# Kernel optimization log

Measured on AMD Instinct MI355X. Metric: run time of the kernel, lower is better.

## Reference

```python
import jax, jax.numpy as jnp
import numpy as np

B, D_IN, D_H, D_OUT, D_INT = 1024, 2048, 4096, 2048, 1024


def fwht(x):
    """Fast Walsh-Hadamard transform over a length-2^k vector (unnormalized),
    faithful to the torch chunk/cat butterfly loop."""
    n = x.shape[0]
    k = int(n).bit_length() - 1
    for i in range(k):
        y = x.reshape(2 ** i, 2, -1)        # split butterfly level i
        x = jnp.stack([y[:, 0] + y[:, 1], y[:, 0] - y[:, 1]], axis=1)
    return x.reshape(n)


def fastfood(V, BB, Pi, GG, DD):
    """fastfood_torched: pad -> B*x -> H -> permute -> G* -> H -> slice/scale."""
    LL = BB.shape[0]
    vpad = jnp.zeros((LL,), V.dtype).at[: V.shape[0]].set(V)
    m5 = fwht(fwht(BB * vpad)[Pi] * GG)
    divisor = jnp.sqrt(LL * jnp.sum(GG * GG))
    return m5[:DD] / (divisor * np.sqrt(float(DD) / LL))


def _ff_vars(key, DD):
    LL = 1 << int(np.ceil(np.log2(DD)))
    k1, k2, k3 = jax.random.split(key, 3)
    BB = jnp.where(jax.random.uniform(k1, (LL,)) < 0.5, -1.0, 1.0).astype(jnp.float32)
    Pi = jax.random.permutation(k2, LL).astype(jnp.int32)
    GG = jax.random.normal(k3, (LL,), dtype=jnp.float32)
    return BB, Pi, GG


def setup_inputs():
    key = jax.random.key(0)
    ks = jax.random.split(key, 8)
    x = jax.random.normal(ks[0], (B, D_IN), dtype=jnp.float32)
    V = jax.random.normal(ks[1], (D_INT,), dtype=jnp.float32) * 0.01
    W1_0 = jax.random.normal(ks[2], (D_H, D_IN), dtype=jnp.float32) * 0.02
    b1_0 = jnp.zeros((D_H,), jnp.float32)
    W2_0 = jax.random.normal(ks[3], (D_OUT, D_H), dtype=jnp.float32) * 0.02
    b2_0 = jnp.zeros((D_OUT,), jnp.float32)
    BB_W1, Pi_W1, GG_W1 = _ff_vars(ks[4], D_H * D_IN)
    BB_b1, Pi_b1, GG_b1 = _ff_vars(ks[5], D_H)
    BB_W2, Pi_W2, GG_W2 = _ff_vars(ks[6], D_OUT * D_H)
    BB_b2, Pi_b2, GG_b2 = _ff_vars(ks[7], D_OUT)
    return dict(x=x, V=V, W1_0=W1_0, b1_0=b1_0, W2_0=W2_0, b2_0=b2_0,
                BB_W1=BB_W1, Pi_W1=Pi_W1, GG_W1=GG_W1,
                BB_b1=BB_b1, Pi_b1=Pi_b1, GG_b1=GG_b1,
                BB_W2=BB_W2, Pi_W2=Pi_W2, GG_W2=GG_W2,
                BB_b2=BB_b2, Pi_b2=Pi_b2, GG_b2=GG_b2)


def reference(x, V, W1_0, b1_0, W2_0, b2_0,
              BB_W1, Pi_W1, GG_W1, BB_b1, Pi_b1, GG_b1,
              BB_W2, Pi_W2, GG_W2, BB_b2, Pi_b2, GG_b2):
    # Reconstruct each parameter: theta = theta0 + fastfood(V).view(shape)
    W1 = W1_0 + fastfood(V, BB_W1, Pi_W1, GG_W1, D_H * D_IN).reshape(D_H, D_IN)
    b1 = b1_0 + fastfood(V, BB_b1, Pi_b1, GG_b1, D_H)
    W2 = W2_0 + fastfood(V, BB_W2, Pi_W2, GG_W2, D_OUT * D_H).reshape(D_OUT, D_H)
    b2 = b2_0 + fastfood(V, BB_b2, Pi_b2, GG_b2, D_OUT)
    # Wrapped module forward (2-layer MLP)
    h = jax.nn.relu(x @ W1.T + b1)
    return h @ W2.T + b2
```

## Files before the change

### kernel.cpp

```cpp
#include <hip/hip_runtime.h>
#include <hip/hip_bf16.h>
#include <stdint.h>


typedef __attribute__((ext_vector_type(8))) short bf16x8;
typedef __attribute__((ext_vector_type(8))) short short8;
typedef __attribute__((ext_vector_type(4))) float f32x4;

__device__ __forceinline__ ushort f2bf(float f) {
  union { float f; uint32_t u; } v; v.f = f;
  return (ushort)((v.u + 0x7FFFu + ((v.u >> 16) & 1u)) >> 16);
}
__device__ __forceinline__ float bf2f(ushort u) {
  union { uint32_t u; float f; } v; v.u = (uint32_t)u << 16; return v.f;
}

__device__ __forceinline__ void gload_lds16(const void* g, void* l) {
  __builtin_amdgcn_global_load_lds(
      (const __attribute__((address_space(1))) void*)g,
      (__attribute__((address_space(3))) void*)l, 16, 0, 0);
}

__device__ __forceinline__ void wait_vm16() { asm volatile("s_waitcnt vmcnt(16)" ::: "memory"); }
__device__ __forceinline__ void wait_vm8()  { asm volatile("s_waitcnt vmcnt(8)"  ::: "memory"); }
__device__ __forceinline__ void wait_vm0()  { asm volatile("s_waitcnt vmcnt(0)"  ::: "memory"); }
__device__ __forceinline__ void wait_lgkm0(){ asm volatile("s_waitcnt lgkmcnt(0)" ::: "memory"); }
__device__ __forceinline__ void barrier_raw(){ asm volatile("s_barrier" ::: "memory"); }

template <int NN>
__device__ __forceinline__ void wht_inreg(float* v) {
#pragma unroll
  for (int h = 1; h < NN; h <<= 1)
#pragma unroll
    for (int g = 0; g < NN; g += (h << 1))
#pragma unroll
      for (int k = 0; k < h; ++k) {
        float a = v[g + k], b = v[g + k + h];
        v[g + k] = a + b; v[g + k + h] = a - b;
      }
}

__global__ __launch_bounds__(256) void prep(
    const float4* __restrict__ x4, ushort4* __restrict__ xb4,
    const float* __restrict__ V,
    const float* __restrict__ BBW1, const float* __restrict__ BBW2,
    float* __restrict__ t1, float* __restrict__ t2,
    const float* __restrict__ BBb1, const int* __restrict__ Pib1,
    const float* __restrict__ GGb1, const float* __restrict__ b10,
    const float* __restrict__ BBb2, const int* __restrict__ Pib2,
    const float* __restrict__ GGb2, const float* __restrict__ b20,
    float* __restrict__ ob1, float* __restrict__ ob2) {
  __shared__ float ts[1024];
  __shared__ float zs[4096];
  __shared__ float red[4];
  const int bid = blockIdx.x;
  const int tid = threadIdx.x;

  if (bid < 2048) {
    int i = bid * 256 + tid;
    float4 v = x4[i];
    ushort4 o;
    o.x = f2bf(v.x); o.y = f2bf(v.y); o.z = f2bf(v.z); o.w = f2bf(v.w);
    xb4[i] = o;
    return;
  }

  if (bid < 2050) {
    const int which = bid - 2048;
    const float* BB = which ? BBW2 : BBW1;
    float* t = which ? t2 : t1;
    for (int i = tid; i < 1024; i += 256) ts[i] = BB[i] * V[i];
    for (int st = 0; st < 10; ++st) {
      int half = 1 << st;
      __syncthreads();
      for (int j = tid; j < 512; j += 256) {
        int p = ((j >> st) << (st + 1)) | (j & (half - 1));
        float a = ts[p], b = ts[p + half];
        ts[p] = a + b; ts[p + half] = a - b;
      }
    }
    __syncthreads();
    for (int i = tid; i < 1024; i += 256) t[i] = ts[i];
    return;
  }

  {
    const int which = bid - 2050;
    const int L = which ? 2048 : 4096;
    const float* BB = which ? BBb2 : BBb1;
    const int* Pi = which ? Pib2 : Pib1;
    const float* GG = which ? GGb2 : GGb1;
    const float* b0 = which ? b20 : b10;
    float* ob = which ? ob2 : ob1;

    for (int i = tid; i < 1024; i += 256) ts[i] = BB[i] * V[i];
    for (int st = 0; st < 10; ++st) {
      int half = 1 << st;
      __syncthreads();
      for (int j = tid; j < 512; j += 256) {
        int p = ((j >> st) << (st + 1)) | (j & (half - 1));
        float a = ts[p], b = ts[p + half];
        ts[p] = a + b; ts[p + half] = a - b;
      }
    }
    __syncthreads();
    float gsum = 0.f;
    for (int i = tid; i < L; i += 256) {
      int pi = Pi[i];
      float g = GG[i];
      gsum += g * g;
      zs[i] = ts[pi & 1023] * g;
    }
    for (int o = 32; o > 0; o >>= 1) gsum += __shfl_down(gsum, o);
    if ((tid & 63) == 0) red[tid >> 6] = gsum;
    __syncthreads();
    float ssum = red[0] + red[1] + red[2] + red[3];
    for (int st = 0; (1 << st) < L; ++st) {
      int half = 1 << st;
      __syncthreads();
      for (int j = tid; j < (L >> 1); j += 256) {
        int p = ((j >> st) << (st + 1)) | (j & (half - 1));
        float a = zs[p], b = zs[p + half];
        zs[p] = a + b; zs[p + half] = a - b;
      }
    }
    __syncthreads();
    float scale = rsqrtf((float)L * ssum);
    for (int i = tid; i < L; i += 256) ob[i] = b0[i] + zs[i] * scale;
  }
}

__global__ __launch_bounds__(256) void build_z(
    const int* __restrict__ Pi1, const float* __restrict__ GG1,
    const int* __restrict__ Pi2, const float* __restrict__ GG2,
    const float* __restrict__ t1, const float* __restrict__ t2,
    ushort* __restrict__ z1, ushort* __restrict__ z2,
    float* __restrict__ partials) {
  __shared__ float ts[1024];
  __shared__ float red[4];
  const int tid = threadIdx.x;
  const int wsel = blockIdx.x >> 10;
  const int blk = blockIdx.x & 1023;
  const int* __restrict__ Pi = wsel ? Pi2 : Pi1;
  const float* __restrict__ GG = wsel ? GG2 : GG1;
  const float* t = wsel ? t2 : t1;
  ushort* __restrict__ z = wsel ? z2 : z1;
  const size_t base = (size_t)blk << 13;

  for (int i = tid; i < 1024; i += 256) ts[i] = t[i];

  int4 p4[8]; float4 g4[8];
  const int4* Pi4 = (const int4*)(Pi + base);
  const float4* GG4 = (const float4*)(GG + base);
#pragma unroll
  for (int q = 0; q < 4; ++q) {
    p4[2 * q]     = Pi4[(q << 9) + (tid << 1)];
    p4[2 * q + 1] = Pi4[(q << 9) + (tid << 1) + 1];
    g4[2 * q]     = GG4[(q << 9) + (tid << 1)];
    g4[2 * q + 1] = GG4[(q << 9) + (tid << 1) + 1];
  }
  __syncthreads();

  float gsum = 0.f;
#pragma unroll
  for (int q = 0; q < 4; ++q) {
    const int4 pa = p4[2 * q], pb = p4[2 * q + 1];
    const float4 ga = g4[2 * q], gb = g4[2 * q + 1];
    gsum += ga.x * ga.x + ga.y * ga.y + ga.z * ga.z + ga.w * ga.w
          + gb.x * gb.x + gb.y * gb.y + gb.z * gb.z + gb.w * gb.w;
    short8 o;
    o[0] = (short)f2bf(ts[pa.x & 1023] * ga.x);
    o[1] = (short)f2bf(ts[pa.y & 1023] * ga.y);
    o[2] = (short)f2bf(ts[pa.z & 1023] * ga.z);
    o[3] = (short)f2bf(ts[pa.w & 1023] * ga.w);
    o[4] = (short)f2bf(ts[pb.x & 1023] * gb.x);
    o[5] = (short)f2bf(ts[pb.y & 1023] * gb.y);
    o[6] = (short)f2bf(ts[pb.z & 1023] * gb.z);
    o[7] = (short)f2bf(ts[pb.w & 1023] * gb.w);
    *(short8*)(z + base + (q << 11) + (tid << 3)) = o;
  }
  for (int o2 = 32; o2 > 0; o2 >>= 1) gsum += __shfl_down(gsum, o2);
  if ((tid & 63) == 0) red[tid >> 6] = gsum;
  __syncthreads();
  if (tid == 0) partials[blockIdx.x] = red[0] + red[1] + red[2] + red[3];
}

__global__ __launch_bounds__(256) void wht13(
    const ushort* __restrict__ zz1, const ushort* __restrict__ zz2,
    ushort* __restrict__ inter1, ushort* __restrict__ inter2) {
  __shared__ float zs[8704];
  const int tid = threadIdx.x;
  const int wsel = blockIdx.x >> 10;
  const int blk = blockIdx.x & 1023;
  const ushort* __restrict__ z = wsel ? zz2 : zz1;
  ushort* __restrict__ inter = wsel ? inter2 : inter1;
  const size_t base = (size_t)blk << 13;

  float v[32];
#pragma unroll
  for (int j = 0; j < 4; ++j) {
    short8 d = *(const short8*)(z + base + (tid << 5) + (j << 3));
#pragma unroll
    for (int k = 0; k < 8; ++k) v[(j << 3) + k] = bf2f((ushort)d[k]);
  }
  wht_inreg<32>(v);
#pragma unroll
  for (int j = 0; j < 16; ++j) {
    float2 u; u.x = v[2 * j]; u.y = v[2 * j + 1];
    *(float2*)&zs[34 * tid + 2 * j] = u;
  }
  __syncthreads();

  {
    const int pb = (tid & 31) + 1088 * (tid >> 5);
#pragma unroll
    for (int r = 0; r < 32; ++r) v[r] = zs[pb + 34 * r];
    wht_inreg<32>(v);
#pragma unroll
    for (int r = 0; r < 32; ++r) zs[pb + 34 * r] = v[r];
  }
  __syncthreads();

  {
    const int pc = 4 * tid + 2 * (tid >> 3);
    float w[4][8];
#pragma unroll
    for (int r = 0; r < 8; ++r) {
      float2 u0 = *(const float2*)&zs[pc + 1088 * r];
      float2 u1 = *(const float2*)&zs[pc + 1088 * r + 2];
      w[0][r] = u0.x; w[1][r] = u0.y; w[2][r] = u1.x; w[3][r] = u1.y;
    }
#pragma unroll
    for (int k = 0; k < 4; ++k) wht_inreg<8>(w[k]);
    ushort* op = inter + base + 4 * tid;
#pragma unroll
    for (int r = 0; r < 8; ++r) {
      short4 o;
      o.x = (short)f2bf(w[0][r]); o.y = (short)f2bf(w[1][r]);
      o.z = (short)f2bf(w[2][r]); o.w = (short)f2bf(w[3][r]);
      *(short4*)&op[r << 10] = o;
    }
  }
}

__global__ __launch_bounds__(512) void ff_pass2(
    const ushort* __restrict__ inter1, const ushort* __restrict__ inter2,
    const float* __restrict__ W01, const float* __restrict__ W02,
    const float* __restrict__ partials,
    ushort* __restrict__ W1b, ushort* __restrict__ W2b) {
  __shared__ ushort tile[1024][34];
  __shared__ float red[8];
  const int tid = threadIdx.x;
  const int wsel = blockIdx.x >> 8;
  const int cb = (blockIdx.x & 255) << 5;
  const ushort* inter = wsel ? inter2 : inter1;
  const float* W0 = wsel ? W02 : W01;
  ushort* Wb = wsel ? W2b : W1b;

  float s = partials[(wsel << 10) + tid] + partials[(wsel << 10) + tid + 512];
  for (int o = 32; o > 0; o >>= 1) s += __shfl_down(s, o);
  if ((tid & 63) == 0) red[tid >> 6] = s;

  const int p = tid & 15;
  const int g = tid >> 4;
  const ushort* ip = inter + ((size_t)(g << 5) << 13) + cb + (p << 1);
  float va[32], vb[32];
#pragma unroll
  for (int r = 0; r < 32; ++r) {
    ushort2 u = *(const ushort2*)(ip + ((size_t)r << 13));
    va[r] = bf2f(u.x); vb[r] = bf2f(u.y);
  }
  wht_inreg<32>(va);
  wht_inreg<32>(vb);
#pragma unroll
  for (int r = 0; r < 32; ++r) {
    ushort2 u; u.x = f2bf(va[r]); u.y = f2bf(vb[r]);
    *(ushort2*)&tile[(g << 5) + r][p << 1] = u;
  }
  __syncthreads();
  float ssum = 0.f;
#pragma unroll
  for (int k = 0; k < 8; ++k) ssum += red[k];
  const float sc = rsqrtf(8388608.f * ssum);

  float wa[32], wb[32];
#pragma unroll
  for (int r = 0; r < 32; ++r) {
    ushort2 u = *(const ushort2*)&tile[g + (r << 5)][p << 1];
    wa[r] = bf2f(u.x); wb[r] = bf2f(u.y);
  }
  wht_inreg<32>(wa);
  wht_inreg<32>(wb);
#pragma unroll
  for (int r = 0; r < 32; ++r) {
    size_t m = (((size_t)(g + (r << 5))) << 13) + cb + (p << 1);
    float2 w0 = *(const float2*)(W0 + m);
    ushort2 u;
    u.x = f2bf(wa[r] * sc + w0.x);
    u.y = f2bf(wb[r] * sc + w0.y);
    *(ushort2*)(Wb + m) = u;
  }
}

template <int EPI, int NT>
__global__ __launch_bounds__(256) void gemm_bt(
    const ushort* __restrict__ A, const ushort* __restrict__ B,
    const float* __restrict__ bias, ushort* __restrict__ Cb, float* __restrict__ Cf,
    int M, int N, int K) {
  __shared__ ushort As[4][8192];
  __shared__ ushort Bs[4][8192];
  const int tid = threadIdx.x;
  const int w = tid >> 6, l = tid & 63;
  const int wr = w >> 1, wc = w & 1;
  const int brow = blockIdx.y << 7, bcol = blockIdx.x << 7;
  const int lrow = l >> 3;
  const int csrc = ((l & 7) ^ lrow) << 3;
  const int l15 = l & 15;
  const int x7 = l15 & 7;
  const int kb = blockIdx.z * (NT << 6);
  f32x4 acc[4][4] = {};

  const ushort* pa = A + (size_t)(brow + (w << 5) + lrow) * K + kb + csrc;
  const ushort* pb = B + (size_t)(bcol + (w << 5) + lrow) * K + kb + csrc;
  const size_t K8 = (size_t)K << 3;

#define STAGE(buf, tt)                                                      \
  {                                                                         \
    const ushort* qa = pa + ((tt) << 6);                                    \
    const ushort* qb = pb + ((tt) << 6);                                    \
    _Pragma("unroll")                                                       \
    for (int i = 0; i < 4; ++i) {                                           \
      gload_lds16(qa + K8 * i, &As[buf][(((w << 2) + i) << 9)]);            \
      gload_lds16(qb + K8 * i, &Bs[buf][(((w << 2) + i) << 9)]);            \
    }                                                                       \
  }

  STAGE(0, 0); STAGE(1, 1); STAGE(2, 2);
  for (int t = 0; t < NT; ++t) {
    if (t < NT - 2) wait_vm16();
    else if (t == NT - 2) wait_vm8();
    else wait_vm0();
    barrier_raw();
    if (t + 3 < NT) STAGE((t + 3) & 3, t + 3);
    const ushort* Acur = As[t & 3];
    const ushort* Bcur = Bs[t & 3];
    bf16x8 af[2][4], bfr[2][4];
#pragma unroll
    for (int kk = 0; kk < 2; ++kk) {
      int c8 = (kk << 2) + (l >> 4);
#pragma unroll
      for (int m = 0; m < 4; ++m)
        af[kk][m] = *(const bf16x8*)&Acur[(((wr << 6) + (m << 4) + l15) << 6) + ((c8 ^ x7) << 3)];
#pragma unroll
      for (int n = 0; n < 4; ++n)
        bfr[kk][n] = *(const bf16x8*)&Bcur[(((wc << 6) + (n << 4) + l15) << 6) + ((c8 ^ x7) << 3)];
    }
    wait_lgkm0();
#pragma unroll
    for (int kk = 0; kk < 2; ++kk)
#pragma unroll
      for (int m = 0; m < 4; ++m)
#pragma unroll
        for (int n = 0; n < 4; ++n)
          acc[m][n] = __builtin_amdgcn_mfma_f32_16x16x32_bf16(af[kk][m], bfr[kk][n], acc[m][n], 0, 0, 0);
  }
#undef STAGE

  if (EPI == 0) {
#pragma unroll
    for (int n = 0; n < 4; ++n) {
      int col = bcol + (wc << 6) + (n << 4) + l15;
      float bv = bias[col];
#pragma unroll
      for (int m = 0; m < 4; ++m) {
        int row0 = brow + (wr << 6) + (m << 4) + ((l >> 4) << 2);
#pragma unroll
        for (int j = 0; j < 4; ++j) {
          float vv = fmaxf(acc[m][n][j] + bv, 0.f);
          Cb[(size_t)(row0 + j) * N + col] = f2bf(vv);
        }
      }
    }
  } else {
    float* outp = Cf + (size_t)blockIdx.z * M * N;
#pragma unroll
    for (int n = 0; n < 4; ++n) {
      int col = bcol + (wc << 6) + (n << 4) + l15;
#pragma unroll
      for (int m = 0; m < 4; ++m) {
        int row0 = brow + (wr << 6) + (m << 4) + ((l >> 4) << 2);
#pragma unroll
        for (int j = 0; j < 4; ++j)
          outp[(size_t)(row0 + j) * N + col] = acc[m][n][j];
      }
    }
  }
}

__global__ __launch_bounds__(256) void reduce_out(
    const float4* __restrict__ P, const float* __restrict__ b2,
    float4* __restrict__ out) {
  int i = blockIdx.x * 256 + threadIdx.x;
  float4 a = P[i], b = P[i + 524288];
  const float4 bb = *(const float4*)(b2 + ((i & 511) << 2));
  float4 o;
  o.x = a.x + b.x + bb.x; o.y = a.y + b.y + bb.y;
  o.z = a.z + b.z + bb.z; o.w = a.w + b.w + bb.w;
  out[i] = o;
}

extern "C" void kernel_launch(void* const* d_in, const int* in_sizes, int n_in,
                              void* d_out, int out_size, void* d_ws, size_t ws_size,
                              hipStream_t stream) {
  const float* x     = (const float*)d_in[0];
  const float* V     = (const float*)d_in[1];
  const float* W1_0  = (const float*)d_in[2];
  const float* b1_0  = (const float*)d_in[3];
  const float* W2_0  = (const float*)d_in[4];
  const float* b2_0  = (const float*)d_in[5];
  const float* BB_W1 = (const float*)d_in[6];
  const int*   Pi_W1 = (const int*)d_in[7];
  const float* GG_W1 = (const float*)d_in[8];
  const float* BB_b1 = (const float*)d_in[9];
  const int*   Pi_b1 = (const int*)d_in[10];
  const float* GG_b1 = (const float*)d_in[11];
  const float* BB_W2 = (const float*)d_in[12];
  const int*   Pi_W2 = (const int*)d_in[13];
  const float* GG_W2 = (const float*)d_in[14];
  const float* BB_b2 = (const float*)d_in[15];
  const int*   Pi_b2 = (const int*)d_in[16];
  const float* GG_b2 = (const float*)d_in[17];
  float* out = (float*)d_out;

  const size_t MB = 1048576ull;
  char* ws = (char*)d_ws;
  ushort* inter1 = (ushort*)(ws);
  float*  P      = (float*)(ws);
  ushort* inter2 = (ushort*)(ws + 16 * MB);
  ushort* z1     = (ushort*)(ws + 32 * MB);
  ushort* z2     = (ushort*)(ws + 48 * MB);
  ushort* W1b    = (ushort*)(ws + 32 * MB);
  ushort* W2b    = (ushort*)(ws + 48 * MB);
  ushort* xb     = (ushort*)(ws + 64 * MB);
  ushort* hb     = (ushort*)(ws + 68 * MB);
  char*   S      = ws + 76 * MB;
  float*  t1     = (float*)(S);
  float*  t2     = (float*)(S + 4096);
  float*  b1     = (float*)(S + 8192);
  float*  b2     = (float*)(S + 8192 + 16384);
  float*  parts  = (float*)(S + 8192 + 16384 + 8192);

  prep<<<2052, 256, 0, stream>>>((const float4*)x, (ushort4*)xb, V,
                                 BB_W1, BB_W2, t1, t2,
                                 BB_b1, Pi_b1, GG_b1, b1_0,
                                 BB_b2, Pi_b2, GG_b2, b2_0, b1, b2);

  build_z<<<2048, 256, 0, stream>>>(Pi_W1, GG_W1, Pi_W2, GG_W2, t1, t2,
                                    z1, z2, parts);
  wht13<<<2048, 256, 0, stream>>>(z1, z2, inter1, inter2);
  ff_pass2<<<512, 512, 0, stream>>>(inter1, inter2, W1_0, W2_0, parts, W1b, W2b);

  gemm_bt<0, 32><<<dim3(32, 8, 1), 256, 0, stream>>>(xb, W1b, b1, hb, nullptr, 1024, 4096, 2048);
  gemm_bt<1, 32><<<dim3(16, 8, 2), 256, 0, stream>>>(hb, W2b, nullptr, nullptr, P, 1024, 2048, 4096);
  reduce_out<<<2048, 256, 0, stream>>>((const float4*)P, b2, (float4*)out);
}
```

Baseline: 176.6 us.

## Apply Fastfood deltas via Hadamard-transformed activations instead of materializing weights

Instead of building the full Fastfood weight delta with two length-8M Walsh-Hadamard transforms, the code uses the factorisation of the Hadamard matrix into row and column transforms. Activations are transformed row-wise (x·H), multiplied by the permuted/scaled block matrix Y in an extra GEMM, and transformed again, then added in the GEMM epilogue alongside the plain bf16 base-weight GEMM. This removes the large wht13/ff_pass2 passes and the split-K reduction, but adds two extra GEMMs, several row-WHT kernels and a bf16 rounding of the intermediate delta terms, which changes numerical error. The base weights are now converted to bf16 in the prep kernel.

```diff
diff --git a/kernel.cpp b/kernel.cpp
--- a/kernel.cpp
+++ b/kernel.cpp
@@ -42,6 +42,8 @@
 
 __global__ __launch_bounds__(256) void prep(
     const float4* __restrict__ x4, ushort4* __restrict__ xb4,
+    const float4* __restrict__ W10, ushort4* __restrict__ W1b4,
+    const float4* __restrict__ W20, ushort4* __restrict__ W2b4,
     const float* __restrict__ V,
     const float* __restrict__ BBW1, const float* __restrict__ BBW2,
     float* __restrict__ t1, float* __restrict__ t2,
@@ -56,17 +58,20 @@
   const int bid = blockIdx.x;
   const int tid = threadIdx.x;
 
-  if (bid < 2048) {
-    int i = bid * 256 + tid;
-    float4 v = x4[i];
+  if (bid < 18432) {
+    const float4* src; ushort4* dst; int i;
+    if (bid < 2048)       { src = x4;  dst = xb4;  i = bid * 256 + tid; }
+    else if (bid < 10240) { src = W10; dst = W1b4; i = (bid - 2048) * 256 + tid; }
+    else                  { src = W20; dst = W2b4; i = (bid - 10240) * 256 + tid; }
+    float4 v = src[i];
     ushort4 o;
     o.x = f2bf(v.x); o.y = f2bf(v.y); o.z = f2bf(v.z); o.w = f2bf(v.w);
-    xb4[i] = o;
+    dst[i] = o;
     return;
   }
 
-  if (bid < 2050) {
-    const int which = bid - 2048;
+  if (bid < 18434) {
+    const int which = bid - 18432;
     const float* BB = which ? BBW2 : BBW1;
     float* t = which ? t2 : t1;
     for (int i = tid; i < 1024; i += 256) ts[i] = BB[i] * V[i];
@@ -85,7 +90,7 @@
   }
 
   {
-    const int which = bid - 2050;
+    const int which = bid - 18434;
     const int L = which ? 2048 : 4096;
     const float* BB = which ? BBb2 : BBb1;
     const int* Pi = which ? Pib2 : Pib1;
@@ -131,41 +136,26 @@
 }
 
 __global__ __launch_bounds__(256) void build_z(
-    const int* __restrict__ Pi1, const float* __restrict__ GG1,
-    const int* __restrict__ Pi2, const float* __restrict__ GG2,
-    const float* __restrict__ t1, const float* __restrict__ t2,
-    ushort* __restrict__ z1, ushort* __restrict__ z2,
+    const int* __restrict__ Pi, const float* __restrict__ GG,
+    const float* __restrict__ t, ushort* __restrict__ z,
     float* __restrict__ partials) {
   __shared__ float ts[1024];
   __shared__ float red[4];
   const int tid = threadIdx.x;
-  const int wsel = blockIdx.x >> 10;
-  const int blk = blockIdx.x & 1023;
-  const int* __restrict__ Pi = wsel ? Pi2 : Pi1;
-  const float* __restrict__ GG = wsel ? GG2 : GG1;
-  const float* t = wsel ? t2 : t1;
-  ushort* __restrict__ z = wsel ? z2 : z1;
-  const size_t base = (size_t)blk << 13;
+  const size_t base = (size_t)blockIdx.x << 13;
 
   for (int i = tid; i < 1024; i += 256) ts[i] = t[i];
-
-  int4 p4[8]; float4 g4[8];
+  __syncthreads();
+
   const int4* Pi4 = (const int4*)(Pi + base);
   const float4* GG4 = (const float4*)(GG + base);
+  float gsum = 0.f;
 #pragma unroll
   for (int q = 0; q < 4; ++q) {
-    p4[2 * q]     = Pi4[(q << 9) + (tid << 1)];
-    p4[2 * q + 1] = Pi4[(q << 9) + (tid << 1) + 1];
-    g4[2 * q]     = GG4[(q << 9) + (tid << 1)];
-    g4[2 * q + 1] = GG4[(q << 9) + (tid << 1) + 1];
-  }
-  __syncthreads();
-
-  float gsum = 0.f;
-#pragma unroll
-  for (int q = 0; q < 4; ++q) {
-    const int4 pa = p4[2 * q], pb = p4[2 * q + 1];
-    const float4 ga = g4[2 * q], gb = g4[2 * q + 1];
+    const int4 pa = Pi4[(q << 9) + (tid << 1)];
+    const int4 pb = Pi4[(q << 9) + (tid << 1) + 1];
+    const float4 ga = GG4[(q << 9) + (tid << 1)];
+    const float4 gb = GG4[(q << 9) + (tid << 1) + 1];
     gsum += ga.x * ga.x + ga.y * ga.y + ga.z * ga.z + ga.w * ga.w
           + gb.x * gb.x + gb.y * gb.y + gb.z * gb.z + gb.w * gb.w;
     short8 o;
@@ -185,127 +175,129 @@
   if (tid == 0) partials[blockIdx.x] = red[0] + red[1] + red[2] + red[3];
 }
 
-__global__ __launch_bounds__(256) void wht13(
-    const ushort* __restrict__ zz1, const ushort* __restrict__ zz2,
-    ushort* __restrict__ inter1, ushort* __restrict__ inter2) {
-  __shared__ float zs[8704];
+template <bool IN_F32, bool OUT_F32, bool SCALE>
+__global__ __launch_bounds__(256) void rowwht2048(
+    const void* __restrict__ in, void* __restrict__ outp,
+    const float* __restrict__ partials) {
+  __shared__ ushort tile[8][2176];
+  __shared__ float red[4];
   const int tid = threadIdx.x;
-  const int wsel = blockIdx.x >> 10;
-  const int blk = blockIdx.x & 1023;
-  const ushort* __restrict__ z = wsel ? zz2 : zz1;
-  ushort* __restrict__ inter = wsel ? inter2 : inter1;
-  const size_t base = (size_t)blk << 13;
-
-  float v[32];
-#pragma unroll
-  for (int j = 0; j < 4; ++j) {
-    short8 d = *(const short8*)(z + base + (tid << 5) + (j << 3));
-#pragma unroll
-    for (int k = 0; k < 8; ++k) v[(j << 3) + k] = bf2f((ushort)d[k]);
-  }
-  wht_inreg<32>(v);
-#pragma unroll
-  for (int j = 0; j < 16; ++j) {
-    float2 u; u.x = v[2 * j]; u.y = v[2 * j + 1];
-    *(float2*)&zs[34 * tid + 2 * j] = u;
+  const int r = tid >> 5;
+  const int k = tid & 31;
+  const int row = (blockIdx.x << 3) + r;
+  if constexpr (SCALE) {
+    float s = partials[tid] + partials[tid + 256] + partials[tid + 512] + partials[tid + 768];
+    for (int o = 32; o > 0; o >>= 1) s += __shfl_down(s, o);
+    if ((tid & 63) == 0) red[tid >> 6] = s;
+  }
+  float v[64];
+  if constexpr (IN_F32) {
+    const float4* ip = (const float4*)((const float*)in + ((size_t)row << 11) + (k << 6));
+#pragma unroll
+    for (int j = 0; j < 16; ++j) {
+      float4 d = ip[j];
+      v[4 * j] = d.x; v[4 * j + 1] = d.y; v[4 * j + 2] = d.z; v[4 * j + 3] = d.w;
+    }
+  } else {
+    const ushort* ip = (const ushort*)in + ((size_t)row << 11) + (k << 6);
+#pragma unroll
+    for (int j = 0; j < 8; ++j) {
+      short8 d = *(const short8*)(ip + (j << 3));
+#pragma unroll
+      for (int e = 0; e < 8; ++e) v[8 * j + e] = bf2f((ushort)d[e]);
+    }
+  }
+  wht_inreg<64>(v);
+  {
+    ushort* tp = &tile[r][68 * k];
+#pragma unroll
+    for (int j = 0; j < 16; ++j) {
+      ushort4 u;
+      u.x = f2bf(v[4 * j]); u.y = f2bf(v[4 * j + 1]);
+      u.z = f2bf(v[4 * j + 2]); u.w = f2bf(v[4 * j + 3]);
+      *(ushort4*)(tp + (j << 2)) = u;
+    }
   }
   __syncthreads();
-
+  float sc = 1.f;
+  if constexpr (SCALE) sc = rsqrtf(8388608.f * (red[0] + red[1] + red[2] + red[3]));
+
+  float va[32], vb[32];
+#pragma unroll
+  for (int m = 0; m < 32; ++m) {
+    ushort2 u = *(const ushort2*)&tile[r][(k << 1) + 68 * m];
+    va[m] = bf2f(u.x); vb[m] = bf2f(u.y);
+  }
+  wht_inreg<32>(va); wht_inreg<32>(vb);
+  if constexpr (OUT_F32) {
+    float* op = (float*)outp + ((size_t)row << 11) + (k << 1);
+#pragma unroll
+    for (int m = 0; m < 32; ++m) {
+      float2 o; o.x = va[m] * sc; o.y = vb[m] * sc;
+      *(float2*)(op + (m << 6)) = o;
+    }
+  } else {
+    ushort* op = (ushort*)outp + ((size_t)row << 11) + (k << 1);
+#pragma unroll
+    for (int m = 0; m < 32; ++m) {
+      ushort2 o; o.x = f2bf(va[m] * sc); o.y = f2bf(vb[m] * sc);
+      *(ushort2*)(op + (m << 6)) = o;
+    }
+  }
+}
+
+template <bool SCALE>
+__global__ __launch_bounds__(256) void rowwht4096(
+    const ushort* __restrict__ in, ushort* __restrict__ outp,
+    const float* __restrict__ partials) {
+  __shared__ ushort tile[4][4352];
+  __shared__ float red[4];
+  const int tid = threadIdx.x;
+  const int r = tid >> 6;
+  const int k = tid & 63;
+  const int row = (blockIdx.x << 2) + r;
+  if constexpr (SCALE) {
+    float s = partials[tid] + partials[tid + 256] + partials[tid + 512] + partials[tid + 768];
+    for (int o = 32; o > 0; o >>= 1) s += __shfl_down(s, o);
+    if ((tid & 63) == 0) red[tid >> 6] = s;
+  }
+  float v[64];
+  const ushort* ip = in + ((size_t)row << 12) + (k << 6);
+#pragma unroll
+  for (int j = 0; j < 8; ++j) {
+    short8 d = *(const short8*)(ip + (j << 3));
+#pragma unroll
+    for (int e = 0; e < 8; ++e) v[8 * j + e] = bf2f((ushort)d[e]);
+  }
+  wht_inreg<64>(v);
   {
-    const int pb = (tid & 31) + 1088 * (tid >> 5);
-#pragma unroll
-    for (int r = 0; r < 32; ++r) v[r] = zs[pb + 34 * r];
-    wht_inreg<32>(v);
-#pragma unroll
-    for (int r = 0; r < 32; ++r) zs[pb + 34 * r] = v[r];
+    ushort* tp = &tile[r][68 * k];
+#pragma unroll
+    for (int j = 0; j < 16; ++j) {
+      ushort4 u;
+      u.x = f2bf(v[4 * j]); u.y = f2bf(v[4 * j + 1]);
+      u.z = f2bf(v[4 * j + 2]); u.w = f2bf(v[4 * j + 3]);
+      *(ushort4*)(tp + (j << 2)) = u;
+    }
   }
   __syncthreads();
-
-  {
-    const int pc = 4 * tid + 2 * (tid >> 3);
-    float w[4][8];
-#pragma unroll
-    for (int r = 0; r < 8; ++r) {
-      float2 u0 = *(const float2*)&zs[pc + 1088 * r];
-      float2 u1 = *(const float2*)&zs[pc + 1088 * r + 2];
-      w[0][r] = u0.x; w[1][r] = u0.y; w[2][r] = u1.x; w[3][r] = u1.y;
-    }
-#pragma unroll
-    for (int k = 0; k < 4; ++k) wht_inreg<8>(w[k]);
-    ushort* op = inter + base + 4 * tid;
-#pragma unroll
-    for (int r = 0; r < 8; ++r) {
-      short4 o;
-      o.x = (short)f2bf(w[0][r]); o.y = (short)f2bf(w[1][r]);
-      o.z = (short)f2bf(w[2][r]); o.w = (short)f2bf(w[3][r]);
-      *(short4*)&op[r << 10] = o;
-    }
-  }
-}
-
-__global__ __launch_bounds__(512) void ff_pass2(
-    const ushort* __restrict__ inter1, const ushort* __restrict__ inter2,
-    const float* __restrict__ W01, const float* __restrict__ W02,
-    const float* __restrict__ partials,
-    ushort* __restrict__ W1b, ushort* __restrict__ W2b) {
-  __shared__ ushort tile[1024][34];
-  __shared__ float red[8];
-  const int tid = threadIdx.x;
-  const int wsel = blockIdx.x >> 8;
-  const int cb = (blockIdx.x & 255) << 5;
-  const ushort* inter = wsel ? inter2 : inter1;
-  const float* W0 = wsel ? W02 : W01;
-  ushort* Wb = wsel ? W2b : W1b;
-
-  float s = partials[(wsel << 10) + tid] + partials[(wsel << 10) + tid + 512];
-  for (int o = 32; o > 0; o >>= 1) s += __shfl_down(s, o);
-  if ((tid & 63) == 0) red[tid >> 6] = s;
-
-  const int p = tid & 15;
-  const int g = tid >> 4;
-  const ushort* ip = inter + ((size_t)(g << 5) << 13) + cb + (p << 1);
-  float va[32], vb[32];
-#pragma unroll
-  for (int r = 0; r < 32; ++r) {
-    ushort2 u = *(const ushort2*)(ip + ((size_t)r << 13));
-    va[r] = bf2f(u.x); vb[r] = bf2f(u.y);
-  }
-  wht_inreg<32>(va);
-  wht_inreg<32>(vb);
-#pragma unroll
-  for (int r = 0; r < 32; ++r) {
-    ushort2 u; u.x = f2bf(va[r]); u.y = f2bf(vb[r]);
-    *(ushort2*)&tile[(g << 5) + r][p << 1] = u;
-  }
-  __syncthreads();
-  float ssum = 0.f;
-#pragma unroll
-  for (int k = 0; k < 8; ++k) ssum += red[k];
-  const float sc = rsqrtf(8388608.f * ssum);
-
-  float wa[32], wb[32];
-#pragma unroll
-  for (int r = 0; r < 32; ++r) {
-    ushort2 u = *(const ushort2*)&tile[g + (r << 5)][p << 1];
-    wa[r] = bf2f(u.x); wb[r] = bf2f(u.y);
-  }
-  wht_inreg<32>(wa);
-  wht_inreg<32>(wb);
-#pragma unroll
-  for (int r = 0; r < 32; ++r) {
-    size_t m = (((size_t)(g + (r << 5))) << 13) + cb + (p << 1);
-    float2 w0 = *(const float2*)(W0 + m);
-    ushort2 u;
-    u.x = f2bf(wa[r] * sc + w0.x);
-    u.y = f2bf(wb[r] * sc + w0.y);
-    *(ushort2*)(Wb + m) = u;
-  }
+  float sc = 1.f;
+  if constexpr (SCALE) sc = rsqrtf(8388608.f * (red[0] + red[1] + red[2] + red[3]));
+
+  float w[64];
+#pragma unroll
+  for (int m = 0; m < 64; ++m) w[m] = bf2f(tile[r][k + 68 * m]);
+  wht_inreg<64>(w);
+  ushort* op = outp + ((size_t)row << 12) + k;
+#pragma unroll
+  for (int m = 0; m < 64; ++m) op[m << 6] = f2bf(w[m] * sc);
 }
 
 template <int EPI, int NT>
 __global__ __launch_bounds__(256) void gemm_bt(
     const ushort* __restrict__ A, const ushort* __restrict__ B,
-    const float* __restrict__ bias, ushort* __restrict__ Cb, float* __restrict__ Cf,
+    const float* __restrict__ bias, const ushort* __restrict__ Waux,
+    ushort* __restrict__ Cb, float* __restrict__ Cf,
     int M, int N, int K) {
   __shared__ ushort As[4][8192];
   __shared__ ushort Bs[4][8192];
@@ -317,11 +309,10 @@
   const int csrc = ((l & 7) ^ lrow) << 3;
   const int l15 = l & 15;
   const int x7 = l15 & 7;
-  const int kb = blockIdx.z * (NT << 6);
   f32x4 acc[4][4] = {};
 
-  const ushort* pa = A + (size_t)(brow + (w << 5) + lrow) * K + kb + csrc;
-  const ushort* pb = B + (size_t)(bcol + (w << 5) + lrow) * K + kb + csrc;
+  const ushort* pa = A + (size_t)(brow + (w << 5) + lrow) * K + csrc;
+  const ushort* pb = B + (size_t)(bcol + (w << 5) + lrow) * K + csrc;
   const size_t K8 = (size_t)K << 3;
 
 #define STAGE(buf, tt)                                                      \
@@ -366,47 +357,27 @@
   }
 #undef STAGE
 
-  if (EPI == 0) {
-#pragma unroll
-    for (int n = 0; n < 4; ++n) {
-      int col = bcol + (wc << 6) + (n << 4) + l15;
-      float bv = bias[col];
-#pragma unroll
-      for (int m = 0; m < 4; ++m) {
-        int row0 = brow + (wr << 6) + (m << 4) + ((l >> 4) << 2);
-#pragma unroll
-        for (int j = 0; j < 4; ++j) {
-          float vv = fmaxf(acc[m][n][j] + bv, 0.f);
-          Cb[(size_t)(row0 + j) * N + col] = f2bf(vv);
+#pragma unroll
+  for (int n = 0; n < 4; ++n) {
+    int col = bcol + (wc << 6) + (n << 4) + l15;
+    float bv = (EPI == 2) ? 0.f : bias[col];
+#pragma unroll
+    for (int m = 0; m < 4; ++m) {
+      int row0 = brow + (wr << 6) + (m << 4) + ((l >> 4) << 2);
+#pragma unroll
+      for (int j = 0; j < 4; ++j) {
+        size_t idx = (size_t)(row0 + j) * N + col;
+        if (EPI == 2) {
+          Cb[idx] = f2bf(acc[m][n][j]);
+        } else if (EPI == 3) {
+          float vv = acc[m][n][j] + bv + bf2f(Waux[idx]);
+          Cb[idx] = f2bf(fmaxf(vv, 0.f));
+        } else {
+          Cf[idx] = acc[m][n][j] + bv + bf2f(Waux[idx]);
         }
       }
     }
-  } else {
-    float* outp = Cf + (size_t)blockIdx.z * M * N;
-#pragma unroll
-    for (int n = 0; n < 4; ++n) {
-      int col = bcol + (wc << 6) + (n << 4) + l15;
-#pragma unroll
-      for (int m = 0; m < 4; ++m) {
-        int row0 = brow + (wr << 6) + (m << 4) + ((l >> 4) << 2);
-#pragma unroll
-        for (int j = 0; j < 4; ++j)
-          outp[(size_t)(row0 + j) * N + col] = acc[m][n][j];
-      }
-    }
-  }
-}
-
-__global__ __launch_bounds__(256) void reduce_out(
-    const float4* __restrict__ P, const float* __restrict__ b2,
-    float4* __restrict__ out) {
-  int i = blockIdx.x * 256 + threadIdx.x;
-  float4 a = P[i], b = P[i + 524288];
-  const float4 bb = *(const float4*)(b2 + ((i & 511) << 2));
-  float4 o;
-  o.x = a.x + b.x + bb.x; o.y = a.y + b.y + bb.y;
-  o.z = a.z + b.z + bb.z; o.w = a.w + b.w + bb.w;
-  out[i] = o;
+  }
 }
 
 extern "C" void kernel_launch(void* const* d_in, const int* in_sizes, int n_in,
@@ -434,33 +405,39 @@
 
   const size_t MB = 1048576ull;
   char* ws = (char*)d_ws;
-  ushort* inter1 = (ushort*)(ws);
-  float*  P      = (float*)(ws);
-  ushort* inter2 = (ushort*)(ws + 16 * MB);
-  ushort* z1     = (ushort*)(ws + 32 * MB);
-  ushort* z2     = (ushort*)(ws + 48 * MB);
-  ushort* W1b    = (ushort*)(ws + 32 * MB);
-  ushort* W2b    = (ushort*)(ws + 48 * MB);
-  ushort* xb     = (ushort*)(ws + 64 * MB);
-  ushort* hb     = (ushort*)(ws + 68 * MB);
-  char*   S      = ws + 76 * MB;
-  float*  t1     = (float*)(S);
-  float*  t2     = (float*)(S + 4096);
-  float*  b1     = (float*)(S + 8192);
-  float*  b2     = (float*)(S + 8192 + 16384);
-  float*  parts  = (float*)(S + 8192 + 16384 + 8192);
-
-  prep<<<2052, 256, 0, stream>>>((const float4*)x, (ushort4*)xb, V,
-                                 BB_W1, BB_W2, t1, t2,
-                                 BB_b1, Pi_b1, GG_b1, b1_0,
-                                 BB_b2, Pi_b2, GG_b2, b2_0, b1, b2);
-
-  build_z<<<2048, 256, 0, stream>>>(Pi_W1, GG_W1, Pi_W2, GG_W2, t1, t2,
-                                    z1, z2, parts);
-  wht13<<<2048, 256, 0, stream>>>(z1, z2, inter1, inter2);
-  ff_pass2<<<512, 512, 0, stream>>>(inter1, inter2, W1_0, W2_0, parts, W1b, W2b);
-
-  gemm_bt<0, 32><<<dim3(32, 8, 1), 256, 0, stream>>>(xb, W1b, b1, hb, nullptr, 1024, 4096, 2048);
-  gemm_bt<1, 32><<<dim3(16, 8, 2), 256, 0, stream>>>(hb, W2b, nullptr, nullptr, P, 1024, 2048, 4096);
-  reduce_out<<<2048, 256, 0, stream>>>((const float4*)P, b2, (float4*)out);
-}
+  ushort* W2b = (ushort*)(ws);
+  ushort* W1b = (ushort*)(ws + 16 * MB);
+  ushort* hH  = (ushort*)(ws + 16 * MB);
+  ushort* w2  = (ushort*)(ws + 24 * MB);
+  ushort* Y   = (ushort*)(ws + 32 * MB);
+  ushort* hb  = (ushort*)(ws + 48 * MB);
+  ushort* v1b = (ushort*)(ws + 56 * MB);
+  ushort* xb  = (ushort*)(ws + 64 * MB);
+  ushort* ub  = (ushort*)(ws + 68 * MB);
+  char*   S   = ws + 72 * MB;
+  float* t1     = (float*)(S);
+  float* t2     = (float*)(S + 4096);
+  float* b1     = (float*)(S + 8192);
+  float* b2     = (float*)(S + 8192 + 16384);
+  float* parts1 = (float*)(S + 8192 + 16384 + 8192);
+  float* parts2 = (float*)(S + 8192 + 16384 + 8192 + 4096);
+  ushort* w1  = v1b;
+  ushort* v2b = ub;
+
+  prep<<<18436, 256, 0, stream>>>((const float4*)x, (ushort4*)xb,
+                                  (const float4*)W1_0, (ushort4*)W1b,
+                                  (const float4*)W2_0, (ushort4*)W2b,
+                                  V, BB_W1, BB_W2, t1, t2,
+                                  BB_b1, Pi_b1, GG_b1, b1_0,
+                                  BB_b2, Pi_b2, GG_b2, b2_0, b1, b2);
+  rowwht2048<true, false, false><<<128, 256, 0, stream>>>(x, ub, nullptr);
+  build_z<<<1024, 256, 0, stream>>>(Pi_W1, GG_W1, t1, Y, parts1);
+  gemm_bt<2, 32><<<dim3(32, 8), 256, 0, stream>>>(ub, Y, nullptr, nullptr, v1b, nullptr, 1024, 4096, 2048);
+  rowwht4096<true><<<256, 256, 0, stream>>>(v1b, w1, parts1);
+  gemm_bt<3, 32><<<dim3(32, 8), 256, 0, stream>>>(xb, W1b, b1, w1, hb, nullptr, 1024, 4096, 2048);
+  build_z<<<1024, 256, 0, stream>>>(Pi_W2, GG_W2, t2, Y, parts2);
+  rowwht4096<false><<<256, 256, 0, stream>>>(hb, hH, nullptr);
+  gemm_bt<2, 64><<<dim3(16, 8), 256, 0, stream>>>(hH, Y, nullptr, nullptr, v2b, nullptr, 1024, 2048, 4096);
+  rowwht2048<false, false, true><<<128, 256, 0, stream>>>(v2b, w2, parts2);
+  gemm_bt<4, 64><<<dim3(16, 8), 256, 0, stream>>>(hb, W2b, b2, w2, nullptr, out, 1024, 2048, 4096);
+}
```

After: 290.3 us. 64.3% more time.
